# Kernel tuning notes

Measured on AMD Instinct MI355X. Metric: run time of the kernel, lower is better.

The kernel has to match this reference:

```python
import jax, jax.numpy as jnp
import numpy as np

N_NODES = 100000


def _gat_conv(x, edge_index, W, att_src, att_dst, bias, concat):
    """PyG-style GATConv (eval mode, self-loops already in edge_index).
    x: [N, F_in], W: [F_in, H*C], att_*: [H, C], bias: [H*C] or [C].
    """
    N = x.shape[0]
    H, C = att_src.shape
    xl = (x @ W).reshape(N, H, C)                      # [N, H, C]
    a_src = jnp.einsum('nhc,hc->nh', xl, att_src)      # [N, H]
    a_dst = jnp.einsum('nhc,hc->nh', xl, att_dst)      # [N, H]
    src, dst = edge_index[0], edge_index[1]
    e = jax.nn.leaky_relu(a_src[src] + a_dst[dst], negative_slope=0.2)  # [E, H]
    # segment softmax over incoming edges per destination node
    e_max = jax.ops.segment_max(e, dst, num_segments=N)                 # [N, H]
    e_exp = jnp.exp(e - e_max[dst])                                     # [E, H]
    denom = jax.ops.segment_sum(e_exp, dst, num_segments=N)             # [N, H]
    alpha = e_exp / (denom[dst] + 1e-16)                                # [E, H]
    msg = xl[src] * alpha[:, :, None]                                   # [E, H, C]
    out = jax.ops.segment_sum(msg, dst, num_segments=N)                 # [N, H, C]
    out = out.reshape(N, H * C) if concat else out.mean(axis=1)
    return out + bias


def setup_inputs() -> dict:
    key = jax.random.key(0)
    ks = jax.random.split(key, 12)
    in_dim, hidden, heads, out_dim = 128, 16, 8, 64
    E = 1600000
    x = jax.random.normal(ks[0], (N_NODES, in_dim), dtype=jnp.float32)
    edge_index = jax.random.randint(ks[1], (2, E), 0, N_NODES, dtype=jnp.int32)
    s1 = 1.0 / np.sqrt(in_dim)
    s2 = 1.0 / np.sqrt(hidden * heads)
    return {
        'x': x,
        'edge_index': edge_index,
        'W1': jax.random.normal(ks[2], (in_dim, heads * hidden), dtype=jnp.float32) * s1,
        'att_src1': jax.random.normal(ks[3], (heads, hidden), dtype=jnp.float32) * 0.1,
        'att_dst1': jax.random.normal(ks[4], (heads, hidden), dtype=jnp.float32) * 0.1,
        'b1': jnp.zeros((heads * hidden,), dtype=jnp.float32),
        'W2': jax.random.normal(ks[5], (heads * hidden, out_dim), dtype=jnp.float32) * s2,
        'att_src2': jax.random.normal(ks[6], (1, out_dim), dtype=jnp.float32) * 0.1,
        'att_dst2': jax.random.normal(ks[7], (1, out_dim), dtype=jnp.float32) * 0.1,
        'b2': jnp.zeros((out_dim,), dtype=jnp.float32),
    }


def reference(x, edge_index, W1, att_src1, att_dst1, b1, W2, att_src2, att_dst2, b2):
    N = x.shape[0]
    # PyG GATConv default add_self_loops=True
    loops = jnp.tile(jnp.arange(N, dtype=edge_index.dtype), (2, 1))
    ei = jnp.concatenate([edge_index, loops], axis=1)
    h = _gat_conv(x, ei, W1, att_src1, att_dst1, b1, concat=True)
    h = jax.nn.elu(h)
    # dropout is identity in eval mode
    out = _gat_conv(h, ei, W2, att_src2, att_dst2, b2, concat=False)
    return out
```

## Files before the change

kernel.cpp:

```cpp
#include <hip/hip_runtime.h>
#include <cmath>

typedef _Float16 half8 __attribute__((ext_vector_type(8)));
typedef float f32x4 __attribute__((ext_vector_type(4)));

#define CAP 48

__device__ __forceinline__ float elu1(float v) {
    return v > 0.f ? v : (__expf(v) - 1.f);
}

__global__ __launch_bounds__(256) void k_build(
    const int* __restrict__ src, const int* __restrict__ dst,
    int* __restrict__ cnt, int* __restrict__ sorted,
    int E, int M, int npc, int SGRP, int GGRP, int R, int GB,
    const float* __restrict__ x, const float* __restrict__ W,
    const float* __restrict__ att_s, const float* __restrict__ att_d,
    _Float16* __restrict__ xlh, float* __restrict__ a_s, float* __restrict__ a_d, int N)
{
    __shared__ _Float16 Wt[128 * 72];
    int t = threadIdx.x;
    int bid = (int)blockIdx.x;
    int grp = bid >> 3;

    bool isg;
    int sgrp, gg;
    if (R >= 2) {
        int k = grp / R;
        isg = ((grp - k * R) == (R - 1)) && (k < GGRP);
        int cg = k < GGRP ? k : GGRP;
        sgrp = grp - cg;
        gg = k;
    } else {
        isg = grp >= SGRP;
        sgrp = grp;
        gg = grp - SGRP;
    }

    if (!isg) {
        int color = bid & 7;
        int lo = color * npc, hi = lo + npc;
        size_t stride = (size_t)SGRP * 256;
        size_t e0 = (size_t)sgrp * 256 + t;
        int sv[8], dv[8];
#pragma unroll
        for (int it = 0; it < 8; it++) {
            size_t e = e0 + (size_t)it * stride;
            int s = 0, d = -1;
            if (e < (size_t)M) {
                if (e < (size_t)E) { s = src[e]; d = dst[e]; }
                else               { s = (int)(e - E); d = s; }
            }
            sv[it] = s; dv[it] = d;
        }
#pragma unroll
        for (int it = 0; it < 8; it++) {
            int d = dv[it];
            if (d >= lo && d < hi) {
                int pos = atomicAdd(&cnt[d], 1);
                if (pos < CAP) sorted[(size_t)d * CAP + pos] = sv[it];
            }
        }
        return;
    }

    int bx = gg * 8 + (bid & 7);
    if (bx >= GB) return;
    int wave = t >> 6, lane = t & 63;
    int cl = lane & 15, quad = lane >> 4;
    int arow = bx * 64 + wave * 16 + cl;
    int rr = arow < N ? arow : N - 1;

    half8 af[4];
#pragma unroll
    for (int ks = 0; ks < 4; ks++) {
        const float4* p = (const float4*)(x + (size_t)rr * 128 + ks * 32 + quad * 8);
        float4 A = p[0], B = p[1];
        af[ks][0] = (_Float16)A.x; af[ks][1] = (_Float16)A.y;
        af[ks][2] = (_Float16)A.z; af[ks][3] = (_Float16)A.w;
        af[ks][4] = (_Float16)B.x; af[ks][5] = (_Float16)B.y;
        af[ks][6] = (_Float16)B.z; af[ks][7] = (_Float16)B.w;
    }

    f32x4 acc[8];
#pragma unroll
    for (int nt = 0; nt < 8; nt++) acc[nt] = (f32x4){0.f, 0.f, 0.f, 0.f};

#pragma unroll
    for (int h = 0; h < 2; h++) {
        if (h) __syncthreads();
        for (int i = t; i < 128 * 64; i += 256) {
            int k0 = i >> 7, n = i & 127;
            Wt[n * 72 + (k0 ^ (((n >> 3) & 7) << 3))] =
                (_Float16)W[(size_t)(h * 64 + k0) * 128 + n];
        }
        __syncthreads();
#pragma unroll
        for (int nt = 0; nt < 8; nt++) {
            int n = nt * 16 + cl;
            int swz = ((n >> 3) & 7) << 3;
#pragma unroll
            for (int ks2 = 0; ks2 < 2; ks2++) {
                half8 bf = *(const half8*)&Wt[n * 72 + ((ks2 * 32 + quad * 8) ^ swz)];
                acc[nt] = __builtin_amdgcn_mfma_f32_16x16x32_f16(
                    af[h * 2 + ks2], bf, acc[nt], 0, 0, 0);
            }
        }
    }

    float asl[8], adl[8];
#pragma unroll
    for (int nt = 0; nt < 8; nt++) {
        asl[nt] = att_s[nt * 16 + cl];
        adl[nt] = att_d[nt * 16 + cl];
    }

    int rbase = bx * 64 + wave * 16 + quad * 4;
#pragma unroll
    for (int r = 0; r < 4; r++) {
        int orow = rbase + r;
        bool ok = orow < N;
#pragma unroll
        for (int nt = 0; nt < 8; nt++) {
            float v = acc[nt][r];
            if (ok) xlh[(size_t)orow * 128 + nt * 16 + cl] = (_Float16)v;
        }
#pragma unroll
        for (int nt = 0; nt < 8; nt++) {
            float ps = acc[nt][r] * asl[nt];
            float pd = acc[nt][r] * adl[nt];
            ps += __shfl_xor(ps, 1); ps += __shfl_xor(ps, 2);
            ps += __shfl_xor(ps, 4); ps += __shfl_xor(ps, 8);
            pd += __shfl_xor(pd, 1); pd += __shfl_xor(pd, 2);
            pd += __shfl_xor(pd, 4); pd += __shfl_xor(pd, 8);
            if (ok && cl == 0) {
                a_s[(size_t)orow * 8 + nt] = ps;
                a_d[(size_t)orow * 8 + nt] = pd;
            }
        }
    }
}

__global__ __launch_bounds__(256) void k_agg1_gemm2(
    const int* __restrict__ cnt, const int* __restrict__ ss,
    const float* __restrict__ as, const float* __restrict__ ad,
    const _Float16* __restrict__ xlh, const float* __restrict__ b1,
    const float* __restrict__ W2,
    const float* __restrict__ att_s2, const float* __restrict__ att_d2,
    _Float16* __restrict__ xl2h, float* __restrict__ a_s2, float* __restrict__ a_d2, int N)
{
    __shared__ _Float16 W2t[64 * 136];
    __shared__ _Float16 Ht[32 * 136];
    __shared__ float asb[2][32], adb[2][32];

    int t = threadIdx.x;

    for (int i = t; i < 128 * 64; i += 256) {
        int k = i >> 6, n = i & 63;
        W2t[n * 136 + k] = (_Float16)W2[i];
    }

    int ln = t >> 3;
    int g = blockIdx.x * 32 + ln;
    int lane8 = t & 7;
    int c = lane8 * 16;
    {
        int gg = g < N ? g : N - 1;
        int deg = cnt[gg]; deg = deg < CAP ? deg : CAP;
        int start = gg * CAP, end = start + deg;
        float adv = ad[(size_t)gg * 8 + lane8];

        float l = 0.f;
        float acc[16];
#pragma unroll
        for (int j = 0; j < 16; j++) acc[j] = 0.f;

        int i = start;
        for (; i + 4 <= end; i += 4) {
            int s0 = ss[i], s1 = ss[i + 1], s2 = ss[i + 2], s3 = ss[i + 3];
            float a0 = as[(size_t)s0 * 8 + lane8];
            float a1 = as[(size_t)s1 * 8 + lane8];
            float a2 = as[(size_t)s2 * 8 + lane8];
            float a3 = as[(size_t)s3 * 8 + lane8];
            const _Float16* p0 = xlh + (size_t)s0 * 128 + c;
            const _Float16* p1 = xlh + (size_t)s1 * 128 + c;
            const _Float16* p2 = xlh + (size_t)s2 * 128 + c;
            const _Float16* p3 = xlh + (size_t)s3 * 128 + c;
            half8 x0a = *(const half8*)p0, x0b = *(const half8*)(p0 + 8);
            half8 x1a = *(const half8*)p1, x1b = *(const half8*)(p1 + 8);
            half8 x2a = *(const half8*)p2, x2b = *(const half8*)(p2 + 8);
            half8 x3a = *(const half8*)p3, x3b = *(const half8*)(p3 + 8);
            float v0 = a0 + adv; v0 = v0 > 0.f ? v0 : 0.2f * v0;
            float v1 = a1 + adv; v1 = v1 > 0.f ? v1 : 0.2f * v1;
            float v2 = a2 + adv; v2 = v2 > 0.f ? v2 : 0.2f * v2;
            float v3 = a3 + adv; v3 = v3 > 0.f ? v3 : 0.2f * v3;
            float w0 = __expf(v0), w1 = __expf(v1);
            float w2 = __expf(v2), w3 = __expf(v3);
            l += (w0 + w1) + (w2 + w3);
#pragma unroll
            for (int j = 0; j < 8; j++) {
                acc[j]     += ((float)x0a[j] * w0 + (float)x1a[j] * w1)
                            + ((float)x2a[j] * w2 + (float)x3a[j] * w3);
                acc[j + 8] += ((float)x0b[j] * w0 + (float)x1b[j] * w1)
                            + ((float)x2b[j] * w2 + (float)x3b[j] * w3);
            }
        }
        for (; i < end; i++) {
            int s0 = ss[i];
            float v0 = as[(size_t)s0 * 8 + lane8] + adv;
            v0 = v0 > 0.f ? v0 : 0.2f * v0;
            float w0 = __expf(v0);
            l += w0;
            const _Float16* p0 = xlh + (size_t)s0 * 128 + c;
            half8 x0a = *(const half8*)p0, x0b = *(const half8*)(p0 + 8);
#pragma unroll
            for (int j = 0; j < 8; j++) {
                acc[j]     += (float)x0a[j] * w0;
                acc[j + 8] += (float)x0b[j] * w0;
            }
        }
        float inv = 1.f / (l + 1e-16f);
        float4 bq[4];
        bq[0] = *(const float4*)(b1 + c);
        bq[1] = *(const float4*)(b1 + c + 4);
        bq[2] = *(const float4*)(b1 + c + 8);
        bq[3] = *(const float4*)(b1 + c + 12);
        const float* bb = (const float*)bq;
        half8 o0, o1;
#pragma unroll
        for (int j = 0; j < 8; j++) {
            o0[j] = (_Float16)elu1(acc[j] * inv + bb[j]);
            o1[j] = (_Float16)elu1(acc[j + 8] * inv + bb[j + 8]);
        }
        *(half8*)&Ht[ln * 136 + c] = o0;
        *(half8*)&Ht[ln * 136 + c + 8] = o1;
    }
    __syncthreads();

    int wave = t >> 6, lane = t & 63;
    int cl = lane & 15, quad = lane >> 4;
    int rt = wave >> 1;
    int half = wave & 1;

    half8 af[4];
#pragma unroll
    for (int ks = 0; ks < 4; ks++)
        af[ks] = *(const half8*)&Ht[(rt * 16 + cl) * 136 + ks * 32 + quad * 8];

    f32x4 acc2[2];
    acc2[0] = (f32x4){0.f, 0.f, 0.f, 0.f};
    acc2[1] = (f32x4){0.f, 0.f, 0.f, 0.f};
    float asl[2], adl[2];
#pragma unroll
    for (int ntl = 0; ntl < 2; ntl++) {
        int n = (half * 2 + ntl) * 16 + cl;
        asl[ntl] = att_s2[n];
        adl[ntl] = att_d2[n];
#pragma unroll
        for (int ks = 0; ks < 4; ks++) {
            half8 bf = *(const half8*)&W2t[n * 136 + ks * 32 + quad * 8];
            acc2[ntl] = __builtin_amdgcn_mfma_f32_16x16x32_f16(af[ks], bf, acc2[ntl], 0, 0, 0);
        }
    }

#pragma unroll
    for (int r = 0; r < 4; r++) {
        int lrow = rt * 16 + quad * 4 + r;
        int orow = blockIdx.x * 32 + lrow;
        bool ok = orow < N;
        float ps = 0.f, pd = 0.f;
#pragma unroll
        for (int ntl = 0; ntl < 2; ntl++) {
            float v = acc2[ntl][r];
            if (ok) xl2h[(size_t)orow * 64 + (half * 2 + ntl) * 16 + cl] = (_Float16)v;
            ps += v * asl[ntl];
            pd += v * adl[ntl];
        }
        ps += __shfl_xor(ps, 1); ps += __shfl_xor(ps, 2);
        ps += __shfl_xor(ps, 4); ps += __shfl_xor(ps, 8);
        pd += __shfl_xor(pd, 1); pd += __shfl_xor(pd, 2);
        pd += __shfl_xor(pd, 4); pd += __shfl_xor(pd, 8);
        if (cl == 0) { asb[half][lrow] = ps; adb[half][lrow] = pd; }
    }
    __syncthreads();
    if (t < 32) {
        int orow = blockIdx.x * 32 + t;
        if (orow < N) {
            a_s2[orow] = asb[0][t] + asb[1][t];
            a_d2[orow] = adb[0][t] + adb[1][t];
        }
    }
}

__global__ __launch_bounds__(256) void k_agg2(
    const int* __restrict__ cnt, const int* __restrict__ ss,
    const float* __restrict__ as, const float* __restrict__ ad,
    const _Float16* __restrict__ xlh, const float* __restrict__ b2,
    float* __restrict__ out, int N)
{
    int t = threadIdx.x;
    int g = (blockIdx.x * 256 + t) >> 3;
    if (g >= N) return;
    int lane = t & 7;
    int c = lane * 8;
    int deg = cnt[g]; deg = deg < CAP ? deg : CAP;
    int start = g * CAP, end = start + deg;
    float adv = ad[g];

    float l = 0.f;
    float acc[8];
#pragma unroll
    for (int j = 0; j < 8; j++) acc[j] = 0.f;

    int i = start;
    for (; i + 8 <= end; i += 8) {
        int sv[8];
#pragma unroll
        for (int u = 0; u < 8; u++) sv[u] = ss[i + u];
        float av[8];
#pragma unroll
        for (int u = 0; u < 8; u++) av[u] = as[sv[u]];
        half8 xv[8];
#pragma unroll
        for (int u = 0; u < 8; u++)
            xv[u] = *(const half8*)(xlh + (size_t)sv[u] * 64 + c);
        float wv[8];
#pragma unroll
        for (int u = 0; u < 8; u++) {
            float v = av[u] + adv;
            v = v > 0.f ? v : 0.2f * v;
            wv[u] = __expf(v);
        }
        l += ((wv[0] + wv[1]) + (wv[2] + wv[3])) + ((wv[4] + wv[5]) + (wv[6] + wv[7]));
#pragma unroll
        for (int j = 0; j < 8; j++) {
            float s01 = (float)xv[0][j] * wv[0] + (float)xv[1][j] * wv[1];
            float s23 = (float)xv[2][j] * wv[2] + (float)xv[3][j] * wv[3];
            float s45 = (float)xv[4][j] * wv[4] + (float)xv[5][j] * wv[5];
            float s67 = (float)xv[6][j] * wv[6] + (float)xv[7][j] * wv[7];
            acc[j] += (s01 + s23) + (s45 + s67);
        }
    }
    for (; i + 4 <= end; i += 4) {
        int s0 = ss[i], s1 = ss[i + 1], s2 = ss[i + 2], s3 = ss[i + 3];
        float a0 = as[s0], a1 = as[s1], a2 = as[s2], a3 = as[s3];
        half8 x0 = *(const half8*)(xlh + (size_t)s0 * 64 + c);
        half8 x1 = *(const half8*)(xlh + (size_t)s1 * 64 + c);
        half8 x2 = *(const half8*)(xlh + (size_t)s2 * 64 + c);
        half8 x3 = *(const half8*)(xlh + (size_t)s3 * 64 + c);
        float v0 = a0 + adv; v0 = v0 > 0.f ? v0 : 0.2f * v0;
        float v1 = a1 + adv; v1 = v1 > 0.f ? v1 : 0.2f * v1;
        float v2 = a2 + adv; v2 = v2 > 0.f ? v2 : 0.2f * v2;
        float v3 = a3 + adv; v3 = v3 > 0.f ? v3 : 0.2f * v3;
        float w0 = __expf(v0), w1 = __expf(v1), w2 = __expf(v2), w3 = __expf(v3);
        l += (w0 + w1) + (w2 + w3);
#pragma unroll
        for (int j = 0; j < 8; j++)
            acc[j] += ((float)x0[j] * w0 + (float)x1[j] * w1)
                    + ((float)x2[j] * w2 + (float)x3[j] * w3);
    }
    for (; i < end; i++) {
        int s0 = ss[i];
        float v0 = as[s0] + adv;
        v0 = v0 > 0.f ? v0 : 0.2f * v0;
        float w0 = __expf(v0);
        l += w0;
        half8 x0 = *(const half8*)(xlh + (size_t)s0 * 64 + c);
#pragma unroll
        for (int j = 0; j < 8; j++) acc[j] += (float)x0[j] * w0;
    }
    float inv = 1.f / (l + 1e-16f);
    float4 b0 = *(const float4*)(b2 + c);
    float4 b4 = *(const float4*)(b2 + c + 4);
    float bb[8] = {b0.x, b0.y, b0.z, b0.w, b4.x, b4.y, b4.z, b4.w};
    float4 o0, o1;
    o0.x = acc[0] * inv + bb[0];
    o0.y = acc[1] * inv + bb[1];
    o0.z = acc[2] * inv + bb[2];
    o0.w = acc[3] * inv + bb[3];
    o1.x = acc[4] * inv + bb[4];
    o1.y = acc[5] * inv + bb[5];
    o1.z = acc[6] * inv + bb[6];
    o1.w = acc[7] * inv + bb[7];
    *(float4*)(out + (size_t)g * 64 + c) = o0;
    *(float4*)(out + (size_t)g * 64 + c + 4) = o1;
}

extern "C" void kernel_launch(void* const* d_in, const int* in_sizes, int n_in,
                              void* d_out, int out_size, void* d_ws, size_t ws_size,
                              hipStream_t stream) {
    const float* x   = (const float*)d_in[0];
    const int*   ei  = (const int*)  d_in[1];
    const float* W1  = (const float*)d_in[2];
    const float* as1 = (const float*)d_in[3];
    const float* ad1 = (const float*)d_in[4];
    const float* b1  = (const float*)d_in[5];
    const float* W2  = (const float*)d_in[6];
    const float* as2 = (const float*)d_in[7];
    const float* ad2 = (const float*)d_in[8];
    const float* b2  = (const float*)d_in[9];

    const int N = in_sizes[0] / 128;
    const int E = in_sizes[1] / 2;
    const int M = E + N;
    const int npc = (N + 7) / 8;
    const int SGRP = (M + 256 * 8 - 1) / (256 * 8);
    const int GB = (N + 63) / 64;
    const int GGRP = (GB + 7) / 8;
    const int Tg = SGRP + GGRP;
    int R = GGRP > 0 ? Tg / GGRP : 0;
    const int* src = ei;
    const int* dst = ei + E;

    float* ws    = (float*)d_ws;
    _Float16* xl1h = (_Float16*)ws;
    float* as1v  = ws   + (size_t)N * 64;
    float* ad1v  = as1v + (size_t)N * 8;
    _Float16* xl2h = (_Float16*)(ad1v + (size_t)N * 8);
    float* as2v  = ad1v + (size_t)N * 8 + (size_t)N * 32;
    float* ad2v  = as2v + (size_t)N;
    int*   cnt   = (int*)(ad2v + (size_t)N);
    int*   sorted= cnt + (size_t)N;
    float* out   = (float*)d_out;

    size_t need = ((size_t)N * (115 + CAP)) * 4;
    if (ws_size < need) return;

    hipMemsetAsync(cnt, 0, (size_t)N * 4, stream);

    k_build<<<Tg * 8, 256, 0, stream>>>(
        src, dst, cnt, sorted, E, M, npc, SGRP, GGRP, R, GB,
        x, W1, as1, ad1, xl1h, as1v, ad1v, N);

    k_agg1_gemm2<<<(N + 31) / 32, 256, 0, stream>>>(
        cnt, sorted, as1v, ad1v, xl1h, b1, W2, as2, ad2, xl2h, as2v, ad2v, N);

    k_agg2 <<<(int)(((size_t)N * 8 + 255) / 256), 256, 0, stream>>>(
        cnt, sorted, as2v, ad2v, xl2h, b2, out, N);
}
```

Measured before the change: 328.8 us.

## Drop 8-way color partitioning of edge scatter; one block per 2048 edges

The build kernel used to read every edge eight times, once per color block, and each block kept only the destinations in its own node range, presumably so atomics and writes to a given region came from related blocks. Now each scatter block reads a contiguous chunk of 2048 edges once and inserts all of them, and the scatter and GEMM blocks are interleaved one by one instead of in groups of eight. This cuts edge index reads to an eighth and removes the redundant filtering. The cost is that atomics and sorted writes become scattered across the whole node range, which may lose locality in L2 and across XCDs.

```diff
diff --git a/kernel.cpp b/kernel.cpp
--- a/kernel.cpp
+++ b/kernel.cpp
@@ -13,7 +13,7 @@
 __global__ __launch_bounds__(256) void k_build(
     const int* __restrict__ src, const int* __restrict__ dst,
     int* __restrict__ cnt, int* __restrict__ sorted,
-    int E, int M, int npc, int SGRP, int GGRP, int R, int GB,
+    int E, int M, int SBLK, int R, int GB,
     const float* __restrict__ x, const float* __restrict__ W,
     const float* __restrict__ att_s, const float* __restrict__ att_d,
     _Float16* __restrict__ xlh, float* __restrict__ a_s, float* __restrict__ a_d, int N)
@@ -21,31 +21,27 @@
     __shared__ _Float16 Wt[128 * 72];
     int t = threadIdx.x;
     int bid = (int)blockIdx.x;
-    int grp = bid >> 3;
-
-    bool isg;
-    int sgrp, gg;
+
+    bool isSc;
+    int sid, gx;
     if (R >= 2) {
-        int k = grp / R;
-        isg = ((grp - k * R) == (R - 1)) && (k < GGRP);
-        int cg = k < GGRP ? k : GGRP;
-        sgrp = grp - cg;
-        gg = k;
+        int q = bid / R, rem = bid - q * R;
+        isSc = (rem == R - 1) && (q < SBLK);
+        int scbefore = q < SBLK ? q : SBLK;
+        sid = q;
+        gx = bid - scbefore;
     } else {
-        isg = grp >= SGRP;
-        sgrp = grp;
-        gg = grp - SGRP;
-    }
-
-    if (!isg) {
-        int color = bid & 7;
-        int lo = color * npc, hi = lo + npc;
-        size_t stride = (size_t)SGRP * 256;
-        size_t e0 = (size_t)sgrp * 256 + t;
+        isSc = bid < SBLK;
+        sid = bid;
+        gx = bid - SBLK;
+    }
+
+    if (isSc) {
+        size_t e0 = (size_t)sid * 2048 + t;
         int sv[8], dv[8];
 #pragma unroll
         for (int it = 0; it < 8; it++) {
-            size_t e = e0 + (size_t)it * stride;
+            size_t e = e0 + (size_t)it * 256;
             int s = 0, d = -1;
             if (e < (size_t)M) {
                 if (e < (size_t)E) { s = src[e]; d = dst[e]; }
@@ -56,7 +52,7 @@
 #pragma unroll
         for (int it = 0; it < 8; it++) {
             int d = dv[it];
-            if (d >= lo && d < hi) {
+            if (d >= 0) {
                 int pos = atomicAdd(&cnt[d], 1);
                 if (pos < CAP) sorted[(size_t)d * CAP + pos] = sv[it];
             }
@@ -64,7 +60,7 @@
         return;
     }
 
-    int bx = gg * 8 + (bid & 7);
+    int bx = gx;
     if (bx >= GB) return;
     int wave = t >> 6, lane = t & 63;
     int cl = lane & 15, quad = lane >> 4;
@@ -403,12 +399,10 @@
     const int N = in_sizes[0] / 128;
     const int E = in_sizes[1] / 2;
     const int M = E + N;
-    const int npc = (N + 7) / 8;
-    const int SGRP = (M + 256 * 8 - 1) / (256 * 8);
+    const int SBLK = (M + 2047) / 2048;
     const int GB = (N + 63) / 64;
-    const int GGRP = (GB + 7) / 8;
-    const int Tg = SGRP + GGRP;
-    int R = GGRP > 0 ? Tg / GGRP : 0;
+    const int T = SBLK + GB;
+    int R = SBLK > 0 ? T / SBLK : 0;
     const int* src = ei;
     const int* dst = ei + E;
 
@@ -428,8 +422,8 @@
 
     hipMemsetAsync(cnt, 0, (size_t)N * 4, stream);
 
-    k_build<<<Tg * 8, 256, 0, stream>>>(
-        src, dst, cnt, sorted, E, M, npc, SGRP, GGRP, R, GB,
+    k_build<<<T, 256, 0, stream>>>(
+        src, dst, cnt, sorted, E, M, SBLK, R, GB,
         x, W1, as1, ad1, xl1h, as1v, ad1v, N);
 
     k_agg1_gemm2<<<(N + 31) / 32, 256, 0, stream>>>(
```

After: 329.0 us. About the same (+0.1%).
